# Performance work log

Measured on AMD Instinct MI355X. Metric: run time of the kernel, lower is better.

Reference implementation:

```python
import jax, jax.numpy as jnp
import numpy as np

# Mamba block dims (config: d_model=1024, expand=2, d_state=16, d_conv=4, dt_rank=auto)
D_MODEL = 1024
D_INNER = 2048
D_STATE = 16
D_CONV = 4
DT_RANK = 64
B_SZ = 2
SEQ = 2048
EPS = 1e-5
DT_MIN, DT_MAX, DT_FLOOR = 0.001, 0.1, 1e-4


def setup_inputs() -> dict:
    key = jax.random.key(0)
    ks = jax.random.split(key, 8)
    s = 0.02  # initializer_range
    # dt_proj bias init: inverse-softplus of dt sampled log-uniform in [dt_min, dt_max]
    dt = jnp.exp(jax.random.uniform(ks[6], (D_INNER,)) * (np.log(DT_MAX) - np.log(DT_MIN)) + np.log(DT_MIN))
    dt = jnp.clip(dt, DT_FLOOR, None)
    inv_dt = dt + jnp.log(-jnp.expm1(-dt))
    A_init = jnp.broadcast_to(jnp.arange(1, D_STATE + 1, dtype=jnp.float32), (D_INNER, D_STATE))
    return {
        "hidden_states": jax.random.normal(ks[0], (B_SZ, SEQ, D_MODEL), jnp.float32),
        "norm_weight": jnp.ones((D_MODEL,), jnp.float32),
        "in_proj_w": jax.random.normal(ks[1], (2 * D_INNER, D_MODEL), jnp.float32) * s,
        "conv_w": jax.random.normal(ks[2], (D_INNER, 1, D_CONV), jnp.float32) * s,
        "conv_b": jnp.zeros((D_INNER,), jnp.float32),
        "x_proj_w": jax.random.normal(ks[3], (DT_RANK + 2 * D_STATE, D_INNER), jnp.float32) * s,
        "dt_proj_w": jax.random.normal(ks[4], (D_INNER, DT_RANK), jnp.float32) * s,
        "dt_proj_b": inv_dt,
        "A_log": jnp.log(A_init),
        "D": jnp.ones((D_INNER,), jnp.float32),
        "out_proj_w": jax.random.normal(ks[5], (D_MODEL, D_INNER), jnp.float32) * s,
    }


def reference(hidden_states, norm_weight, in_proj_w, conv_w, conv_b, x_proj_w,
              dt_proj_w, dt_proj_b, A_log, D, out_proj_w):
    residual = hidden_states
    # RMSNorm
    h = hidden_states * jax.lax.rsqrt(jnp.mean(hidden_states * hidden_states, -1, keepdims=True) + EPS)
    h = h * norm_weight
    # input projection -> x (ssm branch) and z (gate)
    xz = h @ in_proj_w.T                      # [B, L, 2*d_inner]
    x, z = jnp.split(xz, 2, axis=-1)
    # causal depthwise conv over time
    xc = x.transpose(0, 2, 1)                 # [B, d_inner, L]
    xc = jax.lax.conv_general_dilated(
        xc, conv_w, window_strides=(1,), padding=[(D_CONV - 1, 0)],
        feature_group_count=D_INNER, dimension_numbers=("NCH", "OIH", "NCH"))
    xc = xc + conv_b[None, :, None]
    x = jax.nn.silu(xc.transpose(0, 2, 1))    # [B, L, d_inner]
    # data-dependent SSM params
    dbl = x @ x_proj_w.T                      # [B, L, dt_rank + 2*d_state]
    dt_r = dbl[..., :DT_RANK]
    Bm = dbl[..., DT_RANK:DT_RANK + D_STATE]  # [B, L, N]
    Cm = dbl[..., DT_RANK + D_STATE:]         # [B, L, N]
    dt = jax.nn.softplus(dt_r @ dt_proj_w.T + dt_proj_b)  # [B, L, d_inner]
    A = -jnp.exp(A_log)                       # [d_inner, N], negative

    def step(hstate, inputs):
        x_t, dt_t, B_t, C_t = inputs          # [B,d],[B,d],[B,N],[B,N]
        dA = jnp.exp(dt_t[..., None] * A)     # [B, d, N]
        hstate = hstate * dA + (dt_t * x_t)[..., None] * B_t[:, None, :]
        y_t = jnp.einsum("bdn,bn->bd", hstate, C_t)
        return hstate, y_t

    xs = (x.transpose(1, 0, 2), dt.transpose(1, 0, 2),
          Bm.transpose(1, 0, 2), Cm.transpose(1, 0, 2))
    h0 = jnp.zeros((hidden_states.shape[0], D_INNER, D_STATE), x.dtype)
    _, ys = jax.lax.scan(step, h0, xs)        # ys: [L, B, d_inner]
    y = ys.transpose(1, 0, 2) + x * D
    y = y * jax.nn.silu(z)                    # gated output
    return y @ out_proj_w.T + residual
```

## Files before the change

### kernel.cpp

```cpp
#include <hip/hip_runtime.h>
#include <math.h>

#define D_MODEL 1024
#define D_INNER 2048
#define D_STATE 16
#define D_CONV  4
#define DT_RANK 64
#define B_SZ    2
#define SEQ     2048
#define NTOK    (B_SZ*SEQ)
#define DBL_N   (DT_RANK + 2*D_STATE)
#define CHUNK   64
#define NCHUNK  (SEQ/CHUNK)

typedef __attribute__((ext_vector_type(8))) short short8;
typedef __attribute__((ext_vector_type(4))) float f32x4;

__device__ __forceinline__ unsigned short f2bf(float f) {
    union { float f; unsigned int u; } v; v.f = f;
    unsigned int r = v.u + 0x7fff + ((v.u >> 16) & 1);
    return (unsigned short)(r >> 16);
}
__device__ __forceinline__ float bf2f(unsigned short u) {
    union { unsigned int u; float f; } v; v.u = ((unsigned int)u) << 16;
    return v.f;
}

__global__ __launch_bounds__(256) void rmsnorm_kernel(
    const float* __restrict__ h, const float* __restrict__ w, unsigned short* __restrict__ out)
{
    int tok = blockIdx.x;
    const float4* row = (const float4*)(h + (size_t)tok * D_MODEL);
    float4 v = row[threadIdx.x];
    float ss = v.x*v.x + v.y*v.y + v.z*v.z + v.w*v.w;
    #pragma unroll
    for (int off = 32; off >= 1; off >>= 1) ss += __shfl_down(ss, off, 64);
    __shared__ float red[4];
    int wave = threadIdx.x >> 6, lane = threadIdx.x & 63;
    if (lane == 0) red[wave] = ss;
    __syncthreads();
    float tot = red[0] + red[1] + red[2] + red[3];
    float scale = rsqrtf(tot * (1.0f / D_MODEL) + 1e-5f);
    float4 wv = ((const float4*)w)[threadIdx.x];
    ushort4 o;
    o.x = f2bf(v.x * scale * wv.x);
    o.y = f2bf(v.y * scale * wv.y);
    o.z = f2bf(v.z * scale * wv.z);
    o.w = f2bf(v.w * scale * wv.w);
    ((ushort4*)(out + (size_t)tok * D_MODEL))[threadIdx.x] = o;
}

__global__ __launch_bounds__(256) void cast_bf16_kernel(
    const float4* __restrict__ in, ushort4* __restrict__ out, int n4)
{
    int i = blockIdx.x * 256 + threadIdx.x;
    if (i < n4) {
        float4 v = in[i];
        ushort4 o; o.x = f2bf(v.x); o.y = f2bf(v.y); o.z = f2bf(v.z); o.w = f2bf(v.w);
        out[i] = o;
    }
}

__global__ __launch_bounds__(256) void mfma_gemm_kernel(
    const unsigned short* __restrict__ A, int lda,
    const unsigned short* __restrict__ W, int ldw,
    float* __restrict__ C, int ldc,
    int K, int Nmax,
    const float* __restrict__ add, int ldadd)
{
    __shared__ __align__(16) unsigned short As[128 * 32];
    __shared__ __align__(16) unsigned short Bs[128 * 32];
    const int bm = blockIdx.y * 128;
    const int bn = blockIdx.x * 128;
    const int tid = threadIdx.x;
    const int lane = tid & 63;
    const int wave = tid >> 6;
    const int wm = (wave >> 1) * 64;
    const int wn = (wave & 1) * 64;
    const int frow = lane & 15;
    const int quad = lane >> 4;

    f32x4 acc[4][4];
    #pragma unroll
    for (int i = 0; i < 4; ++i)
        #pragma unroll
        for (int j = 0; j < 4; ++j)
            acc[i][j] = (f32x4){0.f, 0.f, 0.f, 0.f};

    for (int k0 = 0; k0 < K; k0 += 32) {
        __syncthreads();
        #pragma unroll
        for (int i = 0; i < 2; ++i) {
            int q = (wave * 2 + i) * 64 + lane;
            int r = q >> 2, cc = q & 3;
            const unsigned short* ga = A + (size_t)(bm + r) * lda + k0 + cc * 8;
            const unsigned short* gb = W + (size_t)(bn + r) * ldw + k0 + cc * 8;
            __builtin_amdgcn_global_load_lds(
                (const __attribute__((address_space(1))) void*)ga,
                (__attribute__((address_space(3))) void*)(As + (wave * 2 + i) * 512),
                16, 0, 0);
            __builtin_amdgcn_global_load_lds(
                (const __attribute__((address_space(1))) void*)gb,
                (__attribute__((address_space(3))) void*)(Bs + (wave * 2 + i) * 512),
                16, 0, 0);
        }
        __syncthreads();
        short8 af[4], bf[4];
        #pragma unroll
        for (int i = 0; i < 4; ++i)
            af[i] = *(const short8*)&As[(wm + i * 16 + frow) * 32 + quad * 8];
        #pragma unroll
        for (int j = 0; j < 4; ++j)
            bf[j] = *(const short8*)&Bs[(wn + j * 16 + frow) * 32 + quad * 8];
        #pragma unroll
        for (int i = 0; i < 4; ++i)
            #pragma unroll
            for (int j = 0; j < 4; ++j)
                acc[i][j] = __builtin_amdgcn_mfma_f32_16x16x32_bf16(
                    af[i], bf[j], acc[i][j], 0, 0, 0);
    }

    #pragma unroll
    for (int i = 0; i < 4; ++i) {
        #pragma unroll
        for (int r = 0; r < 4; ++r) {
            int row = bm + wm + i * 16 + quad * 4 + r;
            #pragma unroll
            for (int j = 0; j < 4; ++j) {
                int col = bn + wn + j * 16 + frow;
                if (col < Nmax) {
                    float v = acc[i][j][r];
                    if (add) v += add[(size_t)row * ldadd + col];
                    C[(size_t)row * ldc + col] = v;
                }
            }
        }
    }
}

__global__ __launch_bounds__(256) void gemm_kernel(
    const float* __restrict__ A, int lda,
    const float* __restrict__ W, int ldw,
    float* __restrict__ C, int ldc,
    int M, int N, int K,
    const float* __restrict__ bias,
    int act)
{
    __shared__ float As[16][65];
    __shared__ float Ws[16][65];
    const int bm = blockIdx.y * 64;
    const int bn = blockIdx.x * 64;
    const int tid = threadIdx.x;
    const int tm = tid >> 4, tn = tid & 15;
    float acc[4][4] = {};
    for (int k0 = 0; k0 < K; k0 += 16) {
        #pragma unroll
        for (int j = 0; j < 4; ++j) {
            int e = tid + j * 256;
            int r = e >> 4, c = e & 15;
            As[c][r] = A[(size_t)(bm + r) * lda + k0 + c];
            int nr = bn + r;
            Ws[c][r] = (nr < N) ? W[(size_t)nr * ldw + k0 + c] : 0.0f;
        }
        __syncthreads();
        #pragma unroll
        for (int kk = 0; kk < 16; ++kk) {
            float a[4], wv[4];
            #pragma unroll
            for (int i = 0; i < 4; ++i) a[i] = As[kk][tm + 16 * i];
            #pragma unroll
            for (int j = 0; j < 4; ++j) wv[j] = Ws[kk][tn + 16 * j];
            #pragma unroll
            for (int i = 0; i < 4; ++i)
                #pragma unroll
                for (int j = 0; j < 4; ++j)
                    acc[i][j] = fmaf(a[i], wv[j], acc[i][j]);
        }
        __syncthreads();
    }
    #pragma unroll
    for (int i = 0; i < 4; ++i) {
        int row = bm + tm + 16 * i;
        #pragma unroll
        for (int j = 0; j < 4; ++j) {
            int col = bn + tn + 16 * j;
            if (col < N) {
                float v = acc[i][j];
                if (bias) v += bias[col];
                if (act == 1) v = (v > 20.0f) ? v : log1pf(__expf(v));
                C[(size_t)row * ldc + col] = v;
            }
        }
    }
}

__global__ __launch_bounds__(256) void conv_silu_kernel(
    const float* __restrict__ xz, const float* __restrict__ cw,
    const float* __restrict__ cb, unsigned short* __restrict__ out_bf)
{
    int idx = blockIdx.x * 256 + threadIdx.x;
    int d = idx & (D_INNER - 1);
    int t = (idx >> 11) & (SEQ - 1);
    int b = idx >> 22;
    const float* xcol = xz + (size_t)b * SEQ * (2 * D_INNER) + d;
    float w0 = cw[d * 4 + 0], w1 = cw[d * 4 + 1], w2 = cw[d * 4 + 2], w3 = cw[d * 4 + 3];
    float acc = cb[d];
    if (t >= 3) acc = fmaf(xcol[(size_t)(t - 3) * (2 * D_INNER)], w0, acc);
    if (t >= 2) acc = fmaf(xcol[(size_t)(t - 2) * (2 * D_INNER)], w1, acc);
    if (t >= 1) acc = fmaf(xcol[(size_t)(t - 1) * (2 * D_INNER)], w2, acc);
    acc = fmaf(xcol[(size_t)t * (2 * D_INNER)], w3, acc);
    float sig = 1.0f / (1.0f + __expf(-acc));
    out_bf[(size_t)(b * SEQ + t) * D_INNER + d] = f2bf(acc * sig);
}

__global__ __launch_bounds__(256) void scan_phase1_kernel(
    const float* __restrict__ dtb, const unsigned short* __restrict__ xconv,
    const float* __restrict__ dbl, const float* __restrict__ A_log,
    float* __restrict__ sum_a, float* __restrict__ sum_h)
{
    const int d = blockIdx.y * 256 + threadIdx.x;
    const int c = blockIdx.x;
    const int b = blockIdx.z;
    const int t0 = c * CHUNK;

    float An[D_STATE];
    bool fast = true;
    #pragma unroll
    for (int n = 0; n < D_STATE; ++n) {
        An[n] = -__expf(A_log[d * D_STATE + n]);
        fast = fast && (fabsf(An[n] + (float)(n + 1)) < 2e-3f);
    }
    const float* dt_p = dtb + ((size_t)b * SEQ + t0) * D_INNER + d;
    const unsigned short* x_p = xconv + ((size_t)b * SEQ + t0) * D_INNER + d;
    const float* Brow = dbl + ((size_t)b * SEQ + t0) * DBL_N + DT_RANK;

    float h[D_STATE];
    #pragma unroll
    for (int n = 0; n < D_STATE; ++n) h[n] = 0.f;
    float sumdt = 0.f;

    if (fast) {
        for (int t = 0; t < CHUNK; ++t) {
            float dt = dt_p[(size_t)t * D_INNER];
            float xv = bf2f(x_p[(size_t)t * D_INNER]);
            const float4* B4 = (const float4*)(Brow + (size_t)t * DBL_N);
            float4 b0 = B4[0], b1 = B4[1], b2 = B4[2], b3 = B4[3];
            float Bv[16] = {b0.x,b0.y,b0.z,b0.w, b1.x,b1.y,b1.z,b1.w,
                            b2.x,b2.y,b2.z,b2.w, b3.x,b3.y,b3.z,b3.w};
            sumdt += dt;
            float e1 = __expf(-dt);
            float dtx = dt * xv;
            float ea = 1.f;
            #pragma unroll
            for (int n = 0; n < D_STATE; ++n) {
                ea *= e1;
                h[n] = fmaf(h[n], ea, dtx * Bv[n]);
            }
        }
    } else {
        for (int t = 0; t < CHUNK; ++t) {
            float dt = dt_p[(size_t)t * D_INNER];
            float xv = bf2f(x_p[(size_t)t * D_INNER]);
            const float4* B4 = (const float4*)(Brow + (size_t)t * DBL_N);
            float4 b0 = B4[0], b1 = B4[1], b2 = B4[2], b3 = B4[3];
            float Bv[16] = {b0.x,b0.y,b0.z,b0.w, b1.x,b1.y,b1.z,b1.w,
                            b2.x,b2.y,b2.z,b2.w, b3.x,b3.y,b3.z,b3.w};
            sumdt += dt;
            float dtx = dt * xv;
            #pragma unroll
            for (int n = 0; n < D_STATE; ++n) {
                float ea = __expf(dt * An[n]);
                h[n] = fmaf(h[n], ea, dtx * Bv[n]);
            }
        }
    }

    float a[D_STATE];
    if (fast) {
        float E = __expf(-sumdt);
        float ea = 1.f;
        #pragma unroll
        for (int n = 0; n < D_STATE; ++n) { ea *= E; a[n] = ea; }
    } else {
        #pragma unroll
        for (int n = 0; n < D_STATE; ++n) a[n] = __expf(An[n] * sumdt);
    }
    size_t base = (((size_t)b * D_INNER + d) * NCHUNK + c) * D_STATE;
    #pragma unroll
    for (int i = 0; i < 4; ++i) {
        ((float4*)(sum_a + base))[i] = (float4){a[4*i], a[4*i+1], a[4*i+2], a[4*i+3]};
        ((float4*)(sum_h + base))[i] = (float4){h[4*i], h[4*i+1], h[4*i+2], h[4*i+3]};
    }
}

__global__ __launch_bounds__(256) void scan_carry_kernel(
    const float* __restrict__ sum_a, float* __restrict__ sum_h)
{
    size_t g = (size_t)blockIdx.x * 256 + threadIdx.x;
    size_t bd = g >> 4;
    int n = (int)(g & 15);
    size_t base = bd * NCHUNK * D_STATE + n;
    float hh = 0.f;
    for (int c = 0; c < NCHUNK; ++c) {
        size_t idx = base + (size_t)c * D_STATE;
        float a = sum_a[idx];
        float hp = sum_h[idx];
        sum_h[idx] = hh;
        hh = fmaf(hh, a, hp);
    }
}

__global__ __launch_bounds__(256) void scan_phase3_kernel(
    const float* __restrict__ dtb, const unsigned short* __restrict__ xconv,
    const float* __restrict__ xz, const float* __restrict__ dbl,
    const float* __restrict__ A_log, const float* __restrict__ Dvec,
    const float* __restrict__ hinit, unsigned short* __restrict__ y)
{
    const int d = blockIdx.y * 256 + threadIdx.x;
    const int c = blockIdx.x;
    const int b = blockIdx.z;
    const int t0 = c * CHUNK;

    float An[D_STATE];
    bool fast = true;
    #pragma unroll
    for (int n = 0; n < D_STATE; ++n) {
        An[n] = -__expf(A_log[d * D_STATE + n]);
        fast = fast && (fabsf(An[n] + (float)(n + 1)) < 2e-3f);
    }
    const float Dd = Dvec[d];
    const float* dt_p = dtb + ((size_t)b * SEQ + t0) * D_INNER + d;
    const unsigned short* x_p = xconv + ((size_t)b * SEQ + t0) * D_INNER + d;
    const float* z_p = xz + ((size_t)b * SEQ + t0) * (2 * D_INNER) + D_INNER + d;
    const float* Brow = dbl + ((size_t)b * SEQ + t0) * DBL_N + DT_RANK;
    unsigned short* y_p = y + ((size_t)b * SEQ + t0) * D_INNER + d;

    size_t base = (((size_t)b * D_INNER + d) * NCHUNK + c) * D_STATE;
    float h[D_STATE];
    #pragma unroll
    for (int i = 0; i < 4; ++i) {
        float4 hv = ((const float4*)(hinit + base))[i];
        h[4*i] = hv.x; h[4*i+1] = hv.y; h[4*i+2] = hv.z; h[4*i+3] = hv.w;
    }

    if (fast) {
        for (int t = 0; t < CHUNK; ++t) {
            float dt = dt_p[(size_t)t * D_INNER];
            float xv = bf2f(x_p[(size_t)t * D_INNER]);
            const float4* B4 = (const float4*)(Brow + (size_t)t * DBL_N);
            float4 b0 = B4[0], b1 = B4[1], b2 = B4[2], b3 = B4[3];
            float4 c0 = B4[4], c1 = B4[5], c2 = B4[6], c3 = B4[7];
            float Bv[16] = {b0.x,b0.y,b0.z,b0.w, b1.x,b1.y,b1.z,b1.w,
                            b2.x,b2.y,b2.z,b2.w, b3.x,b3.y,b3.z,b3.w};
            float Cv[16] = {c0.x,c0.y,c0.z,c0.w, c1.x,c1.y,c1.z,c1.w,
                            c2.x,c2.y,c2.z,c2.w, c3.x,c3.y,c3.z,c3.w};
            float e1 = __expf(-dt);
            float dtx = dt * xv;
            float ea = 1.f, yy = 0.f;
            #pragma unroll
            for (int n = 0; n < D_STATE; ++n) {
                ea *= e1;
                h[n] = fmaf(h[n], ea, dtx * Bv[n]);
                yy = fmaf(h[n], Cv[n], yy);
            }
            float zv = z_p[(size_t)t * (2 * D_INNER)];
            float sig = 1.0f / (1.0f + __expf(-zv));
            y_p[(size_t)t * D_INNER] = f2bf((yy + xv * Dd) * (zv * sig));
        }
    } else {
        for (int t = 0; t < CHUNK; ++t) {
            float dt = dt_p[(size_t)t * D_INNER];
            float xv = bf2f(x_p[(size_t)t * D_INNER]);
            const float4* B4 = (const float4*)(Brow + (size_t)t * DBL_N);
            float4 b0 = B4[0], b1 = B4[1], b2 = B4[2], b3 = B4[3];
            float4 c0 = B4[4], c1 = B4[5], c2 = B4[6], c3 = B4[7];
            float Bv[16] = {b0.x,b0.y,b0.z,b0.w, b1.x,b1.y,b1.z,b1.w,
                            b2.x,b2.y,b2.z,b2.w, b3.x,b3.y,b3.z,b3.w};
            float Cv[16] = {c0.x,c0.y,c0.z,c0.w, c1.x,c1.y,c1.z,c1.w,
                            c2.x,c2.y,c2.z,c2.w, c3.x,c3.y,c3.z,c3.w};
            float dtx = dt * xv;
            float yy = 0.f;
            #pragma unroll
            for (int n = 0; n < D_STATE; ++n) {
                float ea = __expf(dt * An[n]);
                h[n] = fmaf(h[n], ea, dtx * Bv[n]);
                yy = fmaf(h[n], Cv[n], yy);
            }
            float zv = z_p[(size_t)t * (2 * D_INNER)];
            float sig = 1.0f / (1.0f + __expf(-zv));
            y_p[(size_t)t * D_INNER] = f2bf((yy + xv * Dd) * (zv * sig));
        }
    }
}

extern "C" void kernel_launch(void* const* d_in, const int* in_sizes, int n_in,
                              void* d_out, int out_size, void* d_ws, size_t ws_size,
                              hipStream_t stream) {
    const float* hs        = (const float*)d_in[0];
    const float* norm_w    = (const float*)d_in[1];
    const float* in_proj_w = (const float*)d_in[2];
    const float* conv_w    = (const float*)d_in[3];
    const float* conv_b    = (const float*)d_in[4];
    const float* x_proj_w  = (const float*)d_in[5];
    const float* dt_proj_w = (const float*)d_in[6];
    const float* dt_proj_b = (const float*)d_in[7];
    const float* A_log     = (const float*)d_in[8];
    const float* Dvec      = (const float*)d_in[9];
    const float* out_proj_w= (const float*)d_in[10];
    float* out = (float*)d_out;

    float* wsf   = (float*)d_ws;
    float* xz    = wsf;
    float* dbl   = xz    + (size_t)16777216;
    float* dtb   = dbl   + (size_t)393216;
    float* sum_a = dtb   + (size_t)8388608;
    float* sum_h = sum_a + (size_t)2097152;
    unsigned short* hnorm_bf = (unsigned short*)(sum_h + 2097152);
    unsigned short* ybuf_bf  = hnorm_bf + (size_t)4194304;
    unsigned short* wi_bf    = ybuf_bf + (size_t)8388608;
    unsigned short* wo_bf    = wi_bf + (size_t)4194304;
    unsigned short* xconv_bf = wo_bf + (size_t)2097152;
    unsigned short* wx_bf    = xconv_bf + (size_t)8388608;

    cast_bf16_kernel<<<(2 * D_INNER * D_MODEL / 4 + 255) / 256, 256, 0, stream>>>(
        (const float4*)in_proj_w, (ushort4*)wi_bf, 2 * D_INNER * D_MODEL / 4);
    cast_bf16_kernel<<<(D_MODEL * D_INNER / 4 + 255) / 256, 256, 0, stream>>>(
        (const float4*)out_proj_w, (ushort4*)wo_bf, D_MODEL * D_INNER / 4);
    cast_bf16_kernel<<<(DBL_N * D_INNER / 4 + 255) / 256, 256, 0, stream>>>(
        (const float4*)x_proj_w, (ushort4*)wx_bf, DBL_N * D_INNER / 4);

    rmsnorm_kernel<<<NTOK, 256, 0, stream>>>(hs, norm_w, hnorm_bf);
    mfma_gemm_kernel<<<dim3((2 * D_INNER) / 128, NTOK / 128), 256, 0, stream>>>(
        hnorm_bf, D_MODEL, wi_bf, D_MODEL, xz, 2 * D_INNER, D_MODEL, 2 * D_INNER, nullptr, 0);
    conv_silu_kernel<<<(NTOK * D_INNER) / 256, 256, 0, stream>>>(
        xz, conv_w, conv_b, xconv_bf);
    mfma_gemm_kernel<<<dim3(1, NTOK / 128), 256, 0, stream>>>(
        xconv_bf, D_INNER, wx_bf, D_INNER, dbl, DBL_N, D_INNER, DBL_N, nullptr, 0);
    gemm_kernel<<<dim3(32, 64), 256, 0, stream>>>(
        dbl, DBL_N, dt_proj_w, DT_RANK, dtb, D_INNER,
        NTOK, D_INNER, DT_RANK, dt_proj_b, 1);
    scan_phase1_kernel<<<dim3(NCHUNK, D_INNER / 256, B_SZ), 256, 0, stream>>>(
        dtb, xconv_bf, dbl, A_log, sum_a, sum_h);
    scan_carry_kernel<<<(B_SZ * D_INNER * D_STATE) / 256, 256, 0, stream>>>(sum_a, sum_h);
    scan_phase3_kernel<<<dim3(NCHUNK, D_INNER / 256, B_SZ), 256, 0, stream>>>(
        dtb, xconv_bf, xz, dbl, A_log, Dvec, sum_h, ybuf_bf);
    mfma_gemm_kernel<<<dim3(D_MODEL / 128, NTOK / 128), 256, 0, stream>>>(
        ybuf_bf, D_INNER, wo_bf, D_INNER, out, D_MODEL, D_INNER, D_MODEL, hs, D_MODEL);
}
```

Before: 422.1 us.

## Store xz in bf16, split-K x_proj, MFMA dt_proj, swizzle GEMM LDS

New measurement: 403.2 us. -4.5%, faster.

```diff
diff --git a/kernel.cpp b/kernel.cpp
--- a/kernel.cpp
+++ b/kernel.cpp
@@ -65,13 +65,17 @@
     const unsigned short* __restrict__ A, int lda,
     const unsigned short* __restrict__ W, int ldw,
     float* __restrict__ C, int ldc,
-    int K, int Nmax,
-    const float* __restrict__ add, int ldadd)
+    unsigned short* __restrict__ Cbf, int ldcbf,
+    int kLen, int Nmax,
+    const float* __restrict__ bias,
+    const float* __restrict__ add, int ldadd,
+    int act, size_t segStride)
 {
     __shared__ __align__(16) unsigned short As[128 * 32];
     __shared__ __align__(16) unsigned short Bs[128 * 32];
     const int bm = blockIdx.y * 128;
     const int bn = blockIdx.x * 128;
+    const int kBeg = blockIdx.z * kLen;
     const int tid = threadIdx.x;
     const int lane = tid & 63;
     const int wave = tid >> 6;
@@ -79,6 +83,9 @@
     const int wn = (wave & 1) * 64;
     const int frow = lane & 15;
     const int quad = lane >> 4;
+    const int sw = (frow >> 1) & 3;
+
+    if (C) C += blockIdx.z * segStride;
 
     f32x4 acc[4][4];
     #pragma unroll
@@ -87,14 +94,15 @@
         for (int j = 0; j < 4; ++j)
             acc[i][j] = (f32x4){0.f, 0.f, 0.f, 0.f};
 
-    for (int k0 = 0; k0 < K; k0 += 32) {
+    for (int k0 = kBeg; k0 < kBeg + kLen; k0 += 32) {
         __syncthreads();
         #pragma unroll
         for (int i = 0; i < 2; ++i) {
             int q = (wave * 2 + i) * 64 + lane;
-            int r = q >> 2, cc = q & 3;
-            const unsigned short* ga = A + (size_t)(bm + r) * lda + k0 + cc * 8;
-            const unsigned short* gb = W + (size_t)(bn + r) * ldw + k0 + cc * 8;
+            int r = q >> 2, cl = q & 3;
+            int cg = cl ^ ((r >> 1) & 3);
+            const unsigned short* ga = A + (size_t)(bm + r) * lda + k0 + cg * 8;
+            const unsigned short* gb = W + (size_t)(bn + r) * ldw + k0 + cg * 8;
             __builtin_amdgcn_global_load_lds(
                 (const __attribute__((address_space(1))) void*)ga,
                 (__attribute__((address_space(3))) void*)(As + (wave * 2 + i) * 512),
@@ -108,10 +116,10 @@
         short8 af[4], bf[4];
         #pragma unroll
         for (int i = 0; i < 4; ++i)
-            af[i] = *(const short8*)&As[(wm + i * 16 + frow) * 32 + quad * 8];
+            af[i] = *(const short8*)&As[(wm + i * 16 + frow) * 32 + (quad ^ sw) * 8];
         #pragma unroll
         for (int j = 0; j < 4; ++j)
-            bf[j] = *(const short8*)&Bs[(wn + j * 16 + frow) * 32 + quad * 8];
+            bf[j] = *(const short8*)&Bs[(wn + j * 16 + frow) * 32 + (quad ^ sw) * 8];
         #pragma unroll
         for (int i = 0; i < 4; ++i)
             #pragma unroll
@@ -130,85 +138,48 @@
                 int col = bn + wn + j * 16 + frow;
                 if (col < Nmax) {
                     float v = acc[i][j][r];
+                    if (bias) v += bias[col];
+                    if (act == 1) v = (v > 20.0f) ? v : log1pf(__expf(v));
                     if (add) v += add[(size_t)row * ldadd + col];
-                    C[(size_t)row * ldc + col] = v;
+                    if (C)   C[(size_t)row * ldc + col] = v;
+                    if (Cbf) Cbf[(size_t)row * ldcbf + col] = f2bf(v);
                 }
             }
         }
     }
 }
 
-__global__ __launch_bounds__(256) void gemm_kernel(
-    const float* __restrict__ A, int lda,
-    const float* __restrict__ W, int ldw,
-    float* __restrict__ C, int ldc,
-    int M, int N, int K,
-    const float* __restrict__ bias,
-    int act)
-{
-    __shared__ float As[16][65];
-    __shared__ float Ws[16][65];
-    const int bm = blockIdx.y * 64;
-    const int bn = blockIdx.x * 64;
-    const int tid = threadIdx.x;
-    const int tm = tid >> 4, tn = tid & 15;
-    float acc[4][4] = {};
-    for (int k0 = 0; k0 < K; k0 += 16) {
-        #pragma unroll
-        for (int j = 0; j < 4; ++j) {
-            int e = tid + j * 256;
-            int r = e >> 4, c = e & 15;
-            As[c][r] = A[(size_t)(bm + r) * lda + k0 + c];
-            int nr = bn + r;
-            Ws[c][r] = (nr < N) ? W[(size_t)nr * ldw + k0 + c] : 0.0f;
-        }
-        __syncthreads();
-        #pragma unroll
-        for (int kk = 0; kk < 16; ++kk) {
-            float a[4], wv[4];
-            #pragma unroll
-            for (int i = 0; i < 4; ++i) a[i] = As[kk][tm + 16 * i];
-            #pragma unroll
-            for (int j = 0; j < 4; ++j) wv[j] = Ws[kk][tn + 16 * j];
-            #pragma unroll
-            for (int i = 0; i < 4; ++i)
-                #pragma unroll
-                for (int j = 0; j < 4; ++j)
-                    acc[i][j] = fmaf(a[i], wv[j], acc[i][j]);
-        }
-        __syncthreads();
-    }
-    #pragma unroll
-    for (int i = 0; i < 4; ++i) {
-        int row = bm + tm + 16 * i;
-        #pragma unroll
-        for (int j = 0; j < 4; ++j) {
-            int col = bn + tn + 16 * j;
-            if (col < N) {
-                float v = acc[i][j];
-                if (bias) v += bias[col];
-                if (act == 1) v = (v > 20.0f) ? v : log1pf(__expf(v));
-                C[(size_t)row * ldc + col] = v;
-            }
-        }
+__global__ __launch_bounds__(256) void reduce_xproj_kernel(
+    const float* __restrict__ part, float* __restrict__ dbl,
+    unsigned short* __restrict__ dtr)
+{
+    const int N = NTOK * DBL_N;
+    int idx = blockIdx.x * 256 + threadIdx.x;
+    if (idx >= N) return;
+    float s = part[idx] + part[idx + N] + part[idx + 2 * N] + part[idx + 3 * N];
+    dbl[idx] = s;
+    unsigned int col = (unsigned int)idx % DBL_N;
+    if (col < DT_RANK) {
+        unsigned int tok = (unsigned int)idx / DBL_N;
+        dtr[(size_t)tok * DT_RANK + col] = f2bf(s);
     }
 }
 
 __global__ __launch_bounds__(256) void conv_silu_kernel(
-    const float* __restrict__ xz, const float* __restrict__ cw,
+    const unsigned short* __restrict__ xz, const float* __restrict__ cw,
     const float* __restrict__ cb, unsigned short* __restrict__ out_bf)
 {
     int idx = blockIdx.x * 256 + threadIdx.x;
     int d = idx & (D_INNER - 1);
     int t = (idx >> 11) & (SEQ - 1);
     int b = idx >> 22;
-    const float* xcol = xz + (size_t)b * SEQ * (2 * D_INNER) + d;
+    const unsigned short* xcol = xz + (size_t)b * SEQ * (2 * D_INNER) + d;
     float w0 = cw[d * 4 + 0], w1 = cw[d * 4 + 1], w2 = cw[d * 4 + 2], w3 = cw[d * 4 + 3];
     float acc = cb[d];
-    if (t >= 3) acc = fmaf(xcol[(size_t)(t - 3) * (2 * D_INNER)], w0, acc);
-    if (t >= 2) acc = fmaf(xcol[(size_t)(t - 2) * (2 * D_INNER)], w1, acc);
-    if (t >= 1) acc = fmaf(xcol[(size_t)(t - 1) * (2 * D_INNER)], w2, acc);
-    acc = fmaf(xcol[(size_t)t * (2 * D_INNER)], w3, acc);
+    if (t >= 3) acc = fmaf(bf2f(xcol[(size_t)(t - 3) * (2 * D_INNER)]), w0, acc);
+    if (t >= 2) acc = fmaf(bf2f(xcol[(size_t)(t - 2) * (2 * D_INNER)]), w1, acc);
+    if (t >= 1) acc = fmaf(bf2f(xcol[(size_t)(t - 1) * (2 * D_INNER)]), w2, acc);
+    acc = fmaf(bf2f(xcol[(size_t)t * (2 * D_INNER)]), w3, acc);
     float sig = 1.0f / (1.0f + __expf(-acc));
     out_bf[(size_t)(b * SEQ + t) * D_INNER + d] = f2bf(acc * sig);
 }
@@ -312,7 +283,7 @@
 
 __global__ __launch_bounds__(256) void scan_phase3_kernel(
     const float* __restrict__ dtb, const unsigned short* __restrict__ xconv,
-    const float* __restrict__ xz, const float* __restrict__ dbl,
+    const unsigned short* __restrict__ xz, const float* __restrict__ dbl,
     const float* __restrict__ A_log, const float* __restrict__ Dvec,
     const float* __restrict__ hinit, unsigned short* __restrict__ y)
 {
@@ -331,7 +302,7 @@
     const float Dd = Dvec[d];
     const float* dt_p = dtb + ((size_t)b * SEQ + t0) * D_INNER + d;
     const unsigned short* x_p = xconv + ((size_t)b * SEQ + t0) * D_INNER + d;
-    const float* z_p = xz + ((size_t)b * SEQ + t0) * (2 * D_INNER) + D_INNER + d;
+    const unsigned short* z_p = xz + ((size_t)b * SEQ + t0) * (2 * D_INNER) + D_INNER + d;
     const float* Brow = dbl + ((size_t)b * SEQ + t0) * DBL_N + DT_RANK;
     unsigned short* y_p = y + ((size_t)b * SEQ + t0) * D_INNER + d;
 
@@ -363,7 +334,7 @@
                 h[n] = fmaf(h[n], ea, dtx * Bv[n]);
                 yy = fmaf(h[n], Cv[n], yy);
             }
-            float zv = z_p[(size_t)t * (2 * D_INNER)];
+            float zv = bf2f(z_p[(size_t)t * (2 * D_INNER)]);
             float sig = 1.0f / (1.0f + __expf(-zv));
             y_p[(size_t)t * D_INNER] = f2bf((yy + xv * Dd) * (zv * sig));
         }
@@ -386,7 +357,7 @@
                 h[n] = fmaf(h[n], ea, dtx * Bv[n]);
                 yy = fmaf(h[n], Cv[n], yy);
             }
-            float zv = z_p[(size_t)t * (2 * D_INNER)];
+            float zv = bf2f(z_p[(size_t)t * (2 * D_INNER)]);
             float sig = 1.0f / (1.0f + __expf(-zv));
             y_p[(size_t)t * D_INNER] = f2bf((yy + xv * Dd) * (zv * sig));
         }
@@ -409,18 +380,21 @@
     const float* out_proj_w= (const float*)d_in[10];
     float* out = (float*)d_out;
 
-    float* wsf   = (float*)d_ws;
-    float* xz    = wsf;
-    float* dbl   = xz    + (size_t)16777216;
-    float* dtb   = dbl   + (size_t)393216;
-    float* sum_a = dtb   + (size_t)8388608;
-    float* sum_h = sum_a + (size_t)2097152;
-    unsigned short* hnorm_bf = (unsigned short*)(sum_h + 2097152);
+    float* wsf      = (float*)d_ws;
+    float* dbl      = wsf;
+    float* dbl_part = dbl      + (size_t)393216;
+    float* dtb      = dbl_part + (size_t)1572864;
+    float* sum_a    = dtb      + (size_t)8388608;
+    float* sum_h    = sum_a    + (size_t)2097152;
+    unsigned short* xz_bf    = (unsigned short*)(sum_h + 2097152);
+    unsigned short* xconv_bf = xz_bf    + (size_t)16777216;
+    unsigned short* hnorm_bf = xconv_bf + (size_t)8388608;
     unsigned short* ybuf_bf  = hnorm_bf + (size_t)4194304;
-    unsigned short* wi_bf    = ybuf_bf + (size_t)8388608;
-    unsigned short* wo_bf    = wi_bf + (size_t)4194304;
-    unsigned short* xconv_bf = wo_bf + (size_t)2097152;
-    unsigned short* wx_bf    = xconv_bf + (size_t)8388608;
+    unsigned short* wi_bf    = ybuf_bf  + (size_t)8388608;
+    unsigned short* wo_bf    = wi_bf    + (size_t)4194304;
+    unsigned short* wx_bf    = wo_bf    + (size_t)2097152;
+    unsigned short* wdt_bf   = wx_bf    + (size_t)262144;
+    unsigned short* dtr_bf   = wdt_bf   + (size_t)131072;
 
     cast_bf16_kernel<<<(2 * D_INNER * D_MODEL / 4 + 255) / 256, 256, 0, stream>>>(
         (const float4*)in_proj_w, (ushort4*)wi_bf, 2 * D_INNER * D_MODEL / 4);
@@ -428,22 +402,29 @@
         (const float4*)out_proj_w, (ushort4*)wo_bf, D_MODEL * D_INNER / 4);
     cast_bf16_kernel<<<(DBL_N * D_INNER / 4 + 255) / 256, 256, 0, stream>>>(
         (const float4*)x_proj_w, (ushort4*)wx_bf, DBL_N * D_INNER / 4);
+    cast_bf16_kernel<<<(D_INNER * DT_RANK / 4 + 255) / 256, 256, 0, stream>>>(
+        (const float4*)dt_proj_w, (ushort4*)wdt_bf, D_INNER * DT_RANK / 4);
 
     rmsnorm_kernel<<<NTOK, 256, 0, stream>>>(hs, norm_w, hnorm_bf);
     mfma_gemm_kernel<<<dim3((2 * D_INNER) / 128, NTOK / 128), 256, 0, stream>>>(
-        hnorm_bf, D_MODEL, wi_bf, D_MODEL, xz, 2 * D_INNER, D_MODEL, 2 * D_INNER, nullptr, 0);
+        hnorm_bf, D_MODEL, wi_bf, D_MODEL, nullptr, 0, xz_bf, 2 * D_INNER,
+        D_MODEL, 2 * D_INNER, nullptr, nullptr, 0, 0, 0);
     conv_silu_kernel<<<(NTOK * D_INNER) / 256, 256, 0, stream>>>(
-        xz, conv_w, conv_b, xconv_bf);
-    mfma_gemm_kernel<<<dim3(1, NTOK / 128), 256, 0, stream>>>(
-        xconv_bf, D_INNER, wx_bf, D_INNER, dbl, DBL_N, D_INNER, DBL_N, nullptr, 0);
-    gemm_kernel<<<dim3(32, 64), 256, 0, stream>>>(
-        dbl, DBL_N, dt_proj_w, DT_RANK, dtb, D_INNER,
-        NTOK, D_INNER, DT_RANK, dt_proj_b, 1);
+        xz_bf, conv_w, conv_b, xconv_bf);
+    mfma_gemm_kernel<<<dim3(1, NTOK / 128, 4), 256, 0, stream>>>(
+        xconv_bf, D_INNER, wx_bf, D_INNER, dbl_part, DBL_N, nullptr, 0,
+        D_INNER / 4, DBL_N, nullptr, nullptr, 0, 0, (size_t)NTOK * DBL_N);
+    reduce_xproj_kernel<<<(NTOK * DBL_N + 255) / 256, 256, 0, stream>>>(
+        dbl_part, dbl, dtr_bf);
+    mfma_gemm_kernel<<<dim3(D_INNER / 128, NTOK / 128), 256, 0, stream>>>(
+        dtr_bf, DT_RANK, wdt_bf, DT_RANK, dtb, D_INNER, nullptr, 0,
+        DT_RANK, D_INNER, dt_proj_b, nullptr, 0, 1, 0);
     scan_phase1_kernel<<<dim3(NCHUNK, D_INNER / 256, B_SZ), 256, 0, stream>>>(
         dtb, xconv_bf, dbl, A_log, sum_a, sum_h);
     scan_carry_kernel<<<(B_SZ * D_INNER * D_STATE) / 256, 256, 0, stream>>>(sum_a, sum_h);
     scan_phase3_kernel<<<dim3(NCHUNK, D_INNER / 256, B_SZ), 256, 0, stream>>>(
-        dtb, xconv_bf, xz, dbl, A_log, Dvec, sum_h, ybuf_bf);
+        dtb, xconv_bf, xz_bf, dbl, A_log, Dvec, sum_h, ybuf_bf);
     mfma_gemm_kernel<<<dim3(D_MODEL / 128, NTOK / 128), 256, 0, stream>>>(
-        ybuf_bf, D_INNER, wo_bf, D_INNER, out, D_MODEL, D_INNER, D_MODEL, hs, D_MODEL);
-}
+        ybuf_bf, D_INNER, wo_bf, D_INNER, out, D_MODEL, nullptr, 0,
+        D_INNER, D_MODEL, nullptr, hs, D_MODEL, 0, 0);
+}
```
